# Performance work log

Measured on AMD Instinct MI355X. Metric: run time of the kernel, lower is better.

## Reference

```python
import jax, jax.numpy as jnp
import numpy as np

N_CAMS, B, J, H, W = 5, 4, 15, 128, 240
CUBE = (80, 80, 20)
NBINS = CUBE[0] * CUBE[1] * CUBE[2]
EPS = 1e-6


def setup_inputs() -> dict:
    key = jax.random.key(0)
    ks = jax.random.split(key, 8)
    heatmaps = jax.random.uniform(ks[0], (N_CAMS, B, J, H, W), dtype=jnp.float32)
    # cameras: rotations about z, placed so scene depth is positive
    ang = np.linspace(0.0, 2 * np.pi, N_CAMS, endpoint=False)
    Rz = np.stack([np.stack([np.cos(ang), -np.sin(ang), np.zeros(N_CAMS)], -1),
                   np.stack([np.sin(ang), np.cos(ang), np.zeros(N_CAMS)], -1),
                   np.stack([np.zeros(N_CAMS), np.zeros(N_CAMS), np.ones(N_CAMS)], -1)], 1)  # [N,3,3]
    R = jnp.asarray(np.broadcast_to(Rz[:, None], (N_CAMS, B, 3, 3)), dtype=jnp.float32)
    T = jnp.broadcast_to(jnp.asarray([0.0, 0.0, -5000.0], jnp.float32), (N_CAMS, B, 3))
    f = jnp.full((N_CAMS, B, 2), 1000.0, jnp.float32)
    c = jnp.broadcast_to(jnp.asarray([960.0, 540.0], jnp.float32), (N_CAMS, B, 2))
    k = 0.01 * jax.random.normal(ks[1], (N_CAMS, B, 3), dtype=jnp.float32)
    p = 0.001 * jax.random.normal(ks[2], (N_CAMS, B, 2), dtype=jnp.float32)
    image_wh = jnp.broadcast_to(jnp.asarray([1920.0, 1080.0], jnp.float32), (N_CAMS, B, 2))
    grid_center = jnp.asarray([0.0, 0.0, 1000.0], jnp.float32) + \
        50.0 * jax.random.normal(ks[3], (B, 3), dtype=jnp.float32)
    grid_size = jnp.asarray([8000.0, 8000.0, 2000.0], jnp.float32)
    return {"heatmaps": heatmaps, "R": R, "T": T, "f": f, "c": c, "k": k,
            "p": p, "image_wh": image_wh, "grid_center": grid_center,
            "grid_size": grid_size}


def compute_grid(grid_size, center):
    # torch.meshgrid default == indexing='ij'
    ax = [jnp.linspace(-grid_size[i] / 2, grid_size[i] / 2, CUBE[i]) + center[i]
          for i in range(3)]
    gx, gy, gz = jnp.meshgrid(ax[0], ax[1], ax[2], indexing='ij')
    return jnp.stack([gx.ravel(), gy.ravel(), gz.ravel()], axis=1)  # [NBINS,3]


def _bilinear_sample(img, g):
    # img [J,H,W]; g [M,2] normalized coords (x,y), align_corners=True, zero pad
    ix = (g[:, 0] + 1.0) * 0.5 * (W - 1)
    iy = (g[:, 1] + 1.0) * 0.5 * (H - 1)
    x0 = jnp.floor(ix); y0 = jnp.floor(iy)
    x1 = x0 + 1.0; y1 = y0 + 1.0
    wx1 = ix - x0; wx0 = 1.0 - wx1
    wy1 = iy - y0; wy0 = 1.0 - wy1

    def gather(xi, yi):
        valid = ((xi >= 0) & (xi < W) & (yi >= 0) & (yi < H)).astype(img.dtype)
        xc = jnp.clip(xi, 0, W - 1).astype(jnp.int32)
        yc = jnp.clip(yi, 0, H - 1).astype(jnp.int32)
        return img[:, yc, xc] * valid  # [J,M]

    return (gather(x0, y0) * (wx0 * wy0) + gather(x1, y0) * (wx1 * wy0) +
            gather(x0, y1) * (wx0 * wy1) + gather(x1, y1) * (wx1 * wy1))


def reference(heatmaps, R, T, f, c, k, p, image_wh, grid_center, grid_size):
    # world grids per sample: [B, NBINS, 3]
    grids = jax.vmap(lambda ctr: compute_grid(grid_size, ctr))(grid_center)
    # project: xcam = R @ (x - T)
    d = grids[None] - T[:, :, None, :]                      # [N,B,M,3]
    xcam = jnp.einsum('nbij,nbmj->nbmi', R, d)              # [N,B,M,3]
    y = xcam[..., :2] / xcam[..., 2:3]                      # [N,B,M,2]
    r2 = jnp.sum(y * y, axis=-1)                            # [N,B,M]
    radial = 1.0 + k[:, :, None, 0] * r2 + k[:, :, None, 1] * r2**2 \
                 + k[:, :, None, 2] * r2**3
    tan = p[:, :, None, 0] * y[..., 1] + p[:, :, None, 1] * y[..., 0]
    xy = y * (radial + tan)[..., None] + \
        r2[..., None] * jnp.stack([p[..., 1], p[..., 0]], -1)[:, :, None, :]
    pix = xy * f[:, :, None, :] + c[:, :, None, :]          # [N,B,M,2]

    wv = image_wh[:, :, None, 0]
    hv = image_wh[:, :, None, 1]
    bound = ((pix[..., 0] >= 0) & (pix[..., 1] >= 0) &
             (pix[..., 0] < wv) & (pix[..., 1] < hv)).astype(heatmaps.dtype)  # [N,B,M]
    maxwh = jnp.maximum(wv, hv)[..., None]
    pixc = jnp.clip(pix, -1.0, maxwh)
    norm = pixc / (image_wh[:, :, None, :] - 1.0) * 2.0 - 1.0
    norm = jnp.clip(norm, -1.1, 1.1)                        # [N,B,M,2]

    sampled = jax.vmap(jax.vmap(_bilinear_sample))(heatmaps, norm)  # [N,B,J,M]

    num = jnp.sum(sampled * bound[:, :, None, :], axis=0)   # [B,J,M]
    den = jnp.sum(bound, axis=0)[:, None, :] + EPS          # [B,1,M]
    cubes = num / den
    cubes = jnp.where(jnp.isnan(cubes), 0.0, cubes)
    cubes = jnp.clip(cubes, 0.0, 1.0)
    cubes = cubes.reshape(B, J, *CUBE)
    return cubes, grids
```

## Files before the change

### kernel.cpp

```cpp
#include <hip/hip_runtime.h>
#include <hip/hip_fp16.h>

#define NCAMS 5
#define BB 4
#define JJ 15
#define JP 16
#define HH 128
#define WW 240
#define CXX 80
#define CYY 80
#define CZZ 20
#define NBINS 128000
#define HW (HH*WW)
#define CUBES_ELEMS (BB*JJ*NBINS)
#define BLOCK 256
#define BLOCKS_PER_B (NBINS / BLOCK)
#define GRID (BB * BLOCKS_PER_B)
#define WS_NEEDED ((size_t)NCAMS * BB * HW * JP * sizeof(__half))

union F4H { float4 f; __half2 h[4]; };

__global__ __launch_bounds__(BLOCK) void transpose_kernel_h(
    const float* __restrict__ hm, float4* __restrict__ tz)
{
    const int t = blockIdx.x * BLOCK + threadIdx.x;
    const int q = t & 1;
    const int pixnb = t >> 1;
    const int nb = pixnb / HW;
    const int pix = pixnb - nb * HW;
    const float* src = hm + (size_t)nb * JJ * HW + pix;
    const int j0 = q * 8;
    F4H u;
#pragma unroll
    for (int r = 0; r < 4; ++r) {
        const int j = j0 + 2 * r;
        const float lo = src[j * HW];
        const float hi = (j + 1 < JJ) ? src[(j + 1) * HW] : 0.f;
        u.h[r] = __floats2half2_rn(lo, hi);
    }
    tz[t] = u.f;
}

__global__ __launch_bounds__(BLOCK) void project_kernel_h(
    const float4* __restrict__ tz,
    const float* __restrict__ R, const float* __restrict__ T,
    const float* __restrict__ f, const float* __restrict__ c,
    const float* __restrict__ k, const float* __restrict__ p,
    const float* __restrict__ wh,
    const float* __restrict__ gc, const float* __restrict__ gs,
    float* __restrict__ out)
{
    const int tile = ((blockIdx.x & 7) * (GRID / 8)) + (blockIdx.x >> 3);
    const int b = tile / BLOCKS_PER_B;
    const int m = (tile % BLOCKS_PER_B) * BLOCK + threadIdx.x;

    const int i   = m / (CYY * CZZ);
    const int rem = m - i * (CYY * CZZ);
    const int jy  = rem / CZZ;
    const int kz  = rem - jy * CZZ;

    const float gs0 = gs[0], gs1 = gs[1], gs2 = gs[2];
    const float gx = -0.5f * gs0 + (float)i  * (gs0 / (float)(CXX - 1)) + gc[b * 3 + 0];
    const float gy = -0.5f * gs1 + (float)jy * (gs1 / (float)(CYY - 1)) + gc[b * 3 + 1];
    const float gz = -0.5f * gs2 + (float)kz * (gs2 / (float)(CZZ - 1)) + gc[b * 3 + 2];

    float* gout = out + CUBES_ELEMS + ((size_t)b * NBINS + m) * 3;
    gout[0] = gx; gout[1] = gy; gout[2] = gz;

    float num[JP];
#pragma unroll
    for (int j = 0; j < JP; ++j) num[j] = 0.f;
    float den = 0.f;

    for (int n = 0; n < NCAMS; ++n) {
        const int pb = n * BB + b;
        const float* Rp = R + pb * 9;

        const float dx = gx - T[pb * 3 + 0];
        const float dy = gy - T[pb * 3 + 1];
        const float dz = gz - T[pb * 3 + 2];

        const float xc = Rp[0] * dx + Rp[1] * dy + Rp[2] * dz;
        const float yc = Rp[3] * dx + Rp[4] * dy + Rp[5] * dz;
        const float zc = Rp[6] * dx + Rp[7] * dy + Rp[8] * dz;

        const float y0 = xc / zc;
        const float y1 = yc / zc;
        const float r2 = y0 * y0 + y1 * y1;

        const float k0 = k[pb * 3 + 0], k1 = k[pb * 3 + 1], k2 = k[pb * 3 + 2];
        const float radial = 1.f + k0 * r2 + k1 * r2 * r2 + k2 * r2 * r2 * r2;
        const float p0v = p[pb * 2 + 0], p1v = p[pb * 2 + 1];
        const float s = radial + p0v * y1 + p1v * y0;
        const float xy0 = y0 * s + r2 * p1v;
        const float xy1 = y1 * s + r2 * p0v;

        const float pixx = xy0 * f[pb * 2 + 0] + c[pb * 2 + 0];
        const float pixy = xy1 * f[pb * 2 + 1] + c[pb * 2 + 1];

        const float wv = wh[pb * 2 + 0], hv = wh[pb * 2 + 1];
        const bool inb = (pixx >= 0.f) & (pixy >= 0.f) & (pixx < wv) & (pixy < hv);
        if (!inb) continue;
        den += 1.f;

        const float maxwh = fmaxf(wv, hv);
        float pcx = fminf(fmaxf(pixx, -1.f), maxwh);
        float pcy = fminf(fmaxf(pixy, -1.f), maxwh);
        float nx = fminf(fmaxf(pcx / (wv - 1.f) * 2.f - 1.f, -1.1f), 1.1f);
        float ny = fminf(fmaxf(pcy / (hv - 1.f) * 2.f - 1.f, -1.1f), 1.1f);

        const float ix = (nx + 1.f) * 0.5f * (float)(WW - 1);
        const float iy = (ny + 1.f) * 0.5f * (float)(HH - 1);
        const float x0f = floorf(ix), y0f = floorf(iy);
        const float x1f = x0f + 1.f, y1f = y0f + 1.f;
        const float wx1 = ix - x0f, wx0 = 1.f - wx1;
        const float wy1 = iy - y0f, wy0 = 1.f - wy1;

        const float vx0 = (x0f >= 0.f && x0f < (float)WW) ? 1.f : 0.f;
        const float vx1 = (x1f >= 0.f && x1f < (float)WW) ? 1.f : 0.f;
        const float vy0 = (y0f >= 0.f && y0f < (float)HH) ? 1.f : 0.f;
        const float vy1 = (y1f >= 0.f && y1f < (float)HH) ? 1.f : 0.f;

        const float w00 = wx0 * wy0 * vx0 * vy0;
        const float w10 = wx1 * wy0 * vx1 * vy0;
        const float w01 = wx0 * wy1 * vx0 * vy1;
        const float w11 = wx1 * wy1 * vx1 * vy1;

        const int xi0 = min(max((int)x0f, 0), WW - 1);
        const int xi1 = min(max((int)x1f, 0), WW - 1);
        const int yi0 = min(max((int)y0f, 0), HH - 1);
        const int yi1 = min(max((int)y1f, 0), HH - 1);

        const float4* img = tz + (size_t)pb * HW * 2;
        const int e00 = (yi0 * WW + xi0) * 2;
        const int e10 = (yi0 * WW + xi1) * 2;
        const int e01 = (yi1 * WW + xi0) * 2;
        const int e11 = (yi1 * WW + xi1) * 2;

        F4H A0, A1, B0, B1, C0, C1, D0, D1;
        A0.f = img[e00]; A1.f = img[e00 + 1];
        B0.f = img[e10]; B1.f = img[e10 + 1];
        C0.f = img[e01]; C1.f = img[e01 + 1];
        D0.f = img[e11]; D1.f = img[e11 + 1];

        const __half2 hw00 = __float2half2_rn(w00);
        const __half2 hw10 = __float2half2_rn(w10);
        const __half2 hw01 = __float2half2_rn(w01);
        const __half2 hw11 = __float2half2_rn(w11);

#pragma unroll
        for (int r = 0; r < 4; ++r) {
            __half2 sA = __hmul2(A0.h[r], hw00);
            sA = __hfma2(B0.h[r], hw10, sA);
            sA = __hfma2(C0.h[r], hw01, sA);
            sA = __hfma2(D0.h[r], hw11, sA);
            const float2 vA = __half22float2(sA);
            num[2 * r + 0] += vA.x;
            num[2 * r + 1] += vA.y;

            __half2 sB = __hmul2(A1.h[r], hw00);
            sB = __hfma2(B1.h[r], hw10, sB);
            sB = __hfma2(C1.h[r], hw01, sB);
            sB = __hfma2(D1.h[r], hw11, sB);
            const float2 vB = __half22float2(sB);
            num[8 + 2 * r + 0] += vB.x;
            num[8 + 2 * r + 1] += vB.y;
        }
    }

    const float inv = 1.f / (den + 1e-6f);
    float* cout = out + (size_t)b * JJ * NBINS + m;
#pragma unroll
    for (int j = 0; j < JJ; ++j) {
        float v = num[j] * inv;
        v = (v != v) ? 0.f : v;
        v = fminf(fmaxf(v, 0.f), 1.f);
        cout[(size_t)j * NBINS] = v;
    }
}

__global__ __launch_bounds__(BLOCK) void project_kernel_fb(
    const float* __restrict__ hm,
    const float* __restrict__ R, const float* __restrict__ T,
    const float* __restrict__ f, const float* __restrict__ c,
    const float* __restrict__ k, const float* __restrict__ p,
    const float* __restrict__ wh,
    const float* __restrict__ gc, const float* __restrict__ gs,
    float* __restrict__ out)
{
    const int b = blockIdx.x / BLOCKS_PER_B;
    const int m = (blockIdx.x % BLOCKS_PER_B) * BLOCK + threadIdx.x;
    const int i   = m / (CYY * CZZ);
    const int rem = m - i * (CYY * CZZ);
    const int jy  = rem / CZZ;
    const int kz  = rem - jy * CZZ;

    const float gs0 = gs[0], gs1 = gs[1], gs2 = gs[2];
    const float gx = -0.5f * gs0 + (float)i  * (gs0 / (float)(CXX - 1)) + gc[b * 3 + 0];
    const float gy = -0.5f * gs1 + (float)jy * (gs1 / (float)(CYY - 1)) + gc[b * 3 + 1];
    const float gz = -0.5f * gs2 + (float)kz * (gs2 / (float)(CZZ - 1)) + gc[b * 3 + 2];

    float* gout = out + CUBES_ELEMS + ((size_t)b * NBINS + m) * 3;
    gout[0] = gx; gout[1] = gy; gout[2] = gz;

    float num[JJ];
#pragma unroll
    for (int j = 0; j < JJ; ++j) num[j] = 0.f;
    float den = 0.f;

    for (int n = 0; n < NCAMS; ++n) {
        const int pb = n * BB + b;
        const float* Rp = R + pb * 9;
        const float dx = gx - T[pb * 3 + 0];
        const float dy = gy - T[pb * 3 + 1];
        const float dz = gz - T[pb * 3 + 2];
        const float xc = Rp[0] * dx + Rp[1] * dy + Rp[2] * dz;
        const float yc = Rp[3] * dx + Rp[4] * dy + Rp[5] * dz;
        const float zc = Rp[6] * dx + Rp[7] * dy + Rp[8] * dz;
        const float y0 = xc / zc;
        const float y1 = yc / zc;
        const float r2 = y0 * y0 + y1 * y1;
        const float k0 = k[pb * 3 + 0], k1 = k[pb * 3 + 1], k2 = k[pb * 3 + 2];
        const float radial = 1.f + k0 * r2 + k1 * r2 * r2 + k2 * r2 * r2 * r2;
        const float p0v = p[pb * 2 + 0], p1v = p[pb * 2 + 1];
        const float s = radial + p0v * y1 + p1v * y0;
        const float xy0 = y0 * s + r2 * p1v;
        const float xy1 = y1 * s + r2 * p0v;
        const float pixx = xy0 * f[pb * 2 + 0] + c[pb * 2 + 0];
        const float pixy = xy1 * f[pb * 2 + 1] + c[pb * 2 + 1];
        const float wv = wh[pb * 2 + 0], hv = wh[pb * 2 + 1];
        const bool inb = (pixx >= 0.f) & (pixy >= 0.f) & (pixx < wv) & (pixy < hv);
        if (!inb) continue;
        den += 1.f;
        const float maxwh = fmaxf(wv, hv);
        float pcx = fminf(fmaxf(pixx, -1.f), maxwh);
        float pcy = fminf(fmaxf(pixy, -1.f), maxwh);
        float nx = fminf(fmaxf(pcx / (wv - 1.f) * 2.f - 1.f, -1.1f), 1.1f);
        float ny = fminf(fmaxf(pcy / (hv - 1.f) * 2.f - 1.f, -1.1f), 1.1f);
        const float ix = (nx + 1.f) * 0.5f * (float)(WW - 1);
        const float iy = (ny + 1.f) * 0.5f * (float)(HH - 1);
        const float x0f = floorf(ix), y0f = floorf(iy);
        const float x1f = x0f + 1.f, y1f = y0f + 1.f;
        const float wx1 = ix - x0f, wx0 = 1.f - wx1;
        const float wy1 = iy - y0f, wy0 = 1.f - wy1;
        const float vx0 = (x0f >= 0.f && x0f < (float)WW) ? 1.f : 0.f;
        const float vx1 = (x1f >= 0.f && x1f < (float)WW) ? 1.f : 0.f;
        const float vy0 = (y0f >= 0.f && y0f < (float)HH) ? 1.f : 0.f;
        const float vy1 = (y1f >= 0.f && y1f < (float)HH) ? 1.f : 0.f;
        const float w00 = wx0 * wy0 * vx0 * vy0;
        const float w10 = wx1 * wy0 * vx1 * vy0;
        const float w01 = wx0 * wy1 * vx0 * vy1;
        const float w11 = wx1 * wy1 * vx1 * vy1;
        const int xi0 = min(max((int)x0f, 0), WW - 1);
        const int xi1 = min(max((int)x1f, 0), WW - 1);
        const int yi0 = min(max((int)y0f, 0), HH - 1);
        const int yi1 = min(max((int)y1f, 0), HH - 1);
        const int o00 = yi0 * WW + xi0;
        const int o10 = yi0 * WW + xi1;
        const int o01 = yi1 * WW + xi0;
        const int o11 = yi1 * WW + xi1;
        const float* img = hm + (size_t)pb * JJ * HW;
#pragma unroll
        for (int j = 0; j < JJ; ++j) {
            const float* pj = img + j * HW;
            num[j] += pj[o00] * w00 + pj[o10] * w10 + pj[o01] * w01 + pj[o11] * w11;
        }
    }

    const float inv = 1.f / (den + 1e-6f);
    float* cout = out + (size_t)b * JJ * NBINS + m;
#pragma unroll
    for (int j = 0; j < JJ; ++j) {
        float v = num[j] * inv;
        v = (v != v) ? 0.f : v;
        v = fminf(fmaxf(v, 0.f), 1.f);
        cout[(size_t)j * NBINS] = v;
    }
}

extern "C" void kernel_launch(void* const* d_in, const int* in_sizes, int n_in,
                              void* d_out, int out_size, void* d_ws, size_t ws_size,
                              hipStream_t stream) {
    const float* hm = (const float*)d_in[0];
    const float* R  = (const float*)d_in[1];
    const float* T  = (const float*)d_in[2];
    const float* f  = (const float*)d_in[3];
    const float* c  = (const float*)d_in[4];
    const float* k  = (const float*)d_in[5];
    const float* p  = (const float*)d_in[6];
    const float* wh = (const float*)d_in[7];
    const float* gc = (const float*)d_in[8];
    const float* gs = (const float*)d_in[9];
    float* out = (float*)d_out;

    if (ws_size >= WS_NEEDED) {
        float4* tz = (float4*)d_ws;
        transpose_kernel_h<<<dim3(NCAMS * BB * HW * 2 / BLOCK), dim3(BLOCK), 0, stream>>>(
            hm, tz);
        project_kernel_h<<<dim3(GRID), dim3(BLOCK), 0, stream>>>(
            tz, R, T, f, c, k, p, wh, gc, gs, out);
    } else {
        project_kernel_fb<<<dim3(GRID), dim3(BLOCK), 0, stream>>>(
            hm, R, T, f, c, k, p, wh, gc, gs, out);
    }
}
```

Measured before the change: 131.0 us.

## Quantize heatmaps to uint8 and accumulate bilinear samples with udot4

```diff
diff --git a/kernel.cpp b/kernel.cpp
--- a/kernel.cpp
+++ b/kernel.cpp
@@ -1,10 +1,8 @@
 #include <hip/hip_runtime.h>
-#include <hip/hip_fp16.h>
 
 #define NCAMS 5
 #define BB 4
 #define JJ 15
-#define JP 16
 #define HH 128
 #define WW 240
 #define CXX 80
@@ -16,33 +14,56 @@
 #define BLOCK 256
 #define BLOCKS_PER_B (NBINS / BLOCK)
 #define GRID (BB * BLOCKS_PER_B)
-#define WS_NEEDED ((size_t)NCAMS * BB * HW * JP * sizeof(__half))
-
-union F4H { float4 f; __half2 h[4]; };
-
-__global__ __launch_bounds__(BLOCK) void transpose_kernel_h(
-    const float* __restrict__ hm, float4* __restrict__ tz)
+#define WS_NEEDED ((size_t)NCAMS * BB * HW * 16)
+
+__device__ __forceinline__ unsigned prm(unsigned a, unsigned b, unsigned s) {
+#if __has_builtin(__builtin_amdgcn_perm)
+    return __builtin_amdgcn_perm(a, b, s);
+#else
+    unsigned long long v = ((unsigned long long)a << 32) | b;
+    unsigned r = 0;
+#pragma unroll
+    for (int i = 0; i < 4; ++i) {
+        unsigned idx = (s >> (8 * i)) & 0xffu;
+        unsigned byte = (idx < 8) ? (unsigned)((v >> (8 * idx)) & 0xff) : 0u;
+        r |= byte << (8 * i);
+    }
+    return r;
+#endif
+}
+
+__device__ __forceinline__ unsigned dot4u8(unsigned a, unsigned b, unsigned c) {
+#if __has_builtin(__builtin_amdgcn_udot4)
+    return __builtin_amdgcn_udot4(a, b, c, false);
+#else
+    return c + (a & 0xff) * (b & 0xff)
+             + ((a >> 8) & 0xff) * ((b >> 8) & 0xff)
+             + ((a >> 16) & 0xff) * ((b >> 16) & 0xff)
+             + (a >> 24) * (b >> 24);
+#endif
+}
+
+__global__ __launch_bounds__(BLOCK) void transpose_kernel_u8(
+    const float* __restrict__ hm, uint4* __restrict__ tz)
 {
     const int t = blockIdx.x * BLOCK + threadIdx.x;
-    const int q = t & 1;
-    const int pixnb = t >> 1;
-    const int nb = pixnb / HW;
-    const int pix = pixnb - nb * HW;
+    const int nb = t / HW;
+    const int pix = t - nb * HW;
     const float* src = hm + (size_t)nb * JJ * HW + pix;
-    const int j0 = q * 8;
-    F4H u;
-#pragma unroll
-    for (int r = 0; r < 4; ++r) {
-        const int j = j0 + 2 * r;
-        const float lo = src[j * HW];
-        const float hi = (j + 1 < JJ) ? src[(j + 1) * HW] : 0.f;
-        u.h[r] = __floats2half2_rn(lo, hi);
-    }
-    tz[t] = u.f;
-}
-
-__global__ __launch_bounds__(BLOCK) void project_kernel_h(
-    const float4* __restrict__ tz,
+    unsigned w[4] = {0u, 0u, 0u, 0u};
+#pragma unroll
+    for (int j = 0; j < JJ; ++j) {
+        const float v = src[j * HW];
+        unsigned u = (unsigned)(v * 255.f + 0.5f);
+        u = u > 255u ? 255u : u;
+        w[j >> 2] |= u << ((j & 3) * 8);
+    }
+    uint4 o; o.x = w[0]; o.y = w[1]; o.z = w[2]; o.w = w[3];
+    tz[t] = o;
+}
+
+__global__ __launch_bounds__(BLOCK) void project_kernel_u8(
+    const uint4* __restrict__ tz,
     const float* __restrict__ R, const float* __restrict__ T,
     const float* __restrict__ f, const float* __restrict__ c,
     const float* __restrict__ k, const float* __restrict__ p,
@@ -67,9 +88,9 @@
     float* gout = out + CUBES_ELEMS + ((size_t)b * NBINS + m) * 3;
     gout[0] = gx; gout[1] = gy; gout[2] = gz;
 
-    float num[JP];
-#pragma unroll
-    for (int j = 0; j < JP; ++j) num[j] = 0.f;
+    unsigned acc[JJ];
+#pragma unroll
+    for (int j = 0; j < JJ; ++j) acc[j] = 0u;
     float den = 0.f;
 
     for (int n = 0; n < NCAMS; ++n) {
@@ -131,49 +152,40 @@
         const int yi0 = min(max((int)y0f, 0), HH - 1);
         const int yi1 = min(max((int)y1f, 0), HH - 1);
 
-        const float4* img = tz + (size_t)pb * HW * 2;
-        const int e00 = (yi0 * WW + xi0) * 2;
-        const int e10 = (yi0 * WW + xi1) * 2;
-        const int e01 = (yi1 * WW + xi0) * 2;
-        const int e11 = (yi1 * WW + xi1) * 2;
-
-        F4H A0, A1, B0, B1, C0, C1, D0, D1;
-        A0.f = img[e00]; A1.f = img[e00 + 1];
-        B0.f = img[e10]; B1.f = img[e10 + 1];
-        C0.f = img[e01]; C1.f = img[e01 + 1];
-        D0.f = img[e11]; D1.f = img[e11 + 1];
-
-        const __half2 hw00 = __float2half2_rn(w00);
-        const __half2 hw10 = __float2half2_rn(w10);
-        const __half2 hw01 = __float2half2_rn(w01);
-        const __half2 hw11 = __float2half2_rn(w11);
-
-#pragma unroll
-        for (int r = 0; r < 4; ++r) {
-            __half2 sA = __hmul2(A0.h[r], hw00);
-            sA = __hfma2(B0.h[r], hw10, sA);
-            sA = __hfma2(C0.h[r], hw01, sA);
-            sA = __hfma2(D0.h[r], hw11, sA);
-            const float2 vA = __half22float2(sA);
-            num[2 * r + 0] += vA.x;
-            num[2 * r + 1] += vA.y;
-
-            __half2 sB = __hmul2(A1.h[r], hw00);
-            sB = __hfma2(B1.h[r], hw10, sB);
-            sB = __hfma2(C1.h[r], hw01, sB);
-            sB = __hfma2(D1.h[r], hw11, sB);
-            const float2 vB = __half22float2(sB);
-            num[8 + 2 * r + 0] += vB.x;
-            num[8 + 2 * r + 1] += vB.y;
+        const uint4* img = tz + (size_t)pb * HW;
+        const uint4 A = img[yi0 * WW + xi0];
+        const uint4 Bc = img[yi0 * WW + xi1];
+        const uint4 Cc = img[yi1 * WW + xi0];
+        const uint4 D = img[yi1 * WW + xi1];
+
+        const unsigned u00 = (unsigned)(w00 * 255.f + 0.5f);
+        const unsigned u10 = (unsigned)(w10 * 255.f + 0.5f);
+        const unsigned u01 = (unsigned)(w01 * 255.f + 0.5f);
+        const unsigned u11 = (unsigned)(w11 * 255.f + 0.5f);
+        const unsigned wp = u00 | (u10 << 8) | (u01 << 16) | (u11 << 24);
+
+        const unsigned Aa[4] = {A.x,  A.y,  A.z,  A.w};
+        const unsigned Ba[4] = {Bc.x, Bc.y, Bc.z, Bc.w};
+        const unsigned Ca[4] = {Cc.x, Cc.y, Cc.z, Cc.w};
+        const unsigned Da[4] = {D.x,  D.y,  D.z,  D.w};
+
+#pragma unroll
+        for (int j = 0; j < JJ; ++j) {
+            const int d = j >> 2;
+            const unsigned bj = (unsigned)(j & 3);
+            const unsigned selAB = 0x0c0c0000u | (bj << 8) | (bj + 4u);
+            const unsigned mAB = prm(Aa[d], Ba[d], selAB);
+            const unsigned mCD = prm(Ca[d], Da[d], selAB);
+            const unsigned bytes = prm(mAB, mCD, 0x01000504u);
+            acc[j] = dot4u8(bytes, wp, acc[j]);
         }
     }
 
-    const float inv = 1.f / (den + 1e-6f);
+    const float inv = 1.f / ((den + 1e-6f) * (255.f * 255.f));
     float* cout = out + (size_t)b * JJ * NBINS + m;
 #pragma unroll
     for (int j = 0; j < JJ; ++j) {
-        float v = num[j] * inv;
-        v = (v != v) ? 0.f : v;
+        float v = (float)acc[j] * inv;
         v = fminf(fmaxf(v, 0.f), 1.f);
         cout[(size_t)j * NBINS] = v;
     }
@@ -294,10 +306,10 @@
     float* out = (float*)d_out;
 
     if (ws_size >= WS_NEEDED) {
-        float4* tz = (float4*)d_ws;
-        transpose_kernel_h<<<dim3(NCAMS * BB * HW * 2 / BLOCK), dim3(BLOCK), 0, stream>>>(
+        uint4* tz = (uint4*)d_ws;
+        transpose_kernel_u8<<<dim3(NCAMS * BB * HW / BLOCK), dim3(BLOCK), 0, stream>>>(
             hm, tz);
-        project_kernel_h<<<dim3(GRID), dim3(BLOCK), 0, stream>>>(
+        project_kernel_u8<<<dim3(GRID), dim3(BLOCK), 0, stream>>>(
             tz, R, T, f, c, k, p, wh, gc, gs, out);
     } else {
         project_kernel_fb<<<dim3(GRID), dim3(BLOCK), 0, stream>>>(
```

New measurement: 119.9 us. 1.09x faster.
